# Kernel tuning notes

Measured on AMD Instinct MI355X. Metric: run time of the kernel, lower is better.

Reference implementation:

```python
import jax, jax.numpy as jnp
import numpy as np

N_NODES = 50000
N_EDGES = 800000
IN_C, HID, OUT_C, N_LAYERS = 32, 64, 8, 3

def _init(key, fan_in, shape):
    return jax.random.normal(key, shape, dtype=jnp.float32) * (1.0 / np.sqrt(fan_in))

def setup_inputs() -> dict:
    key = jax.random.key(0)
    ks = jax.random.split(key, 16)
    x = jax.random.uniform(ks[0], (N_NODES, IN_C), dtype=jnp.float32)
    edge_index = jax.random.randint(ks[1], (2, N_EDGES), 0, N_NODES, dtype=jnp.int64)
    return {
        "x": x,
        "edge_index": edge_index,
        # encoder MLP: in -> hid -> hid
        "enc_w1": _init(ks[2], IN_C, (IN_C, HID)),
        "enc_b1": jnp.zeros((HID,), jnp.float32),
        "enc_w2": _init(ks[3], HID, (HID, HID)),
        "enc_b2": jnp.zeros((HID,), jnp.float32),
        # stacked SAGEConv params: lin_l (aggregated neighbors, has bias) and lin_r (root)
        "sage_wl": _init(ks[4], HID, (N_LAYERS, HID, HID)),
        "sage_wr": _init(ks[5], HID, (N_LAYERS, HID, HID)),
        "sage_b": jnp.zeros((N_LAYERS, HID), jnp.float32),
        # decoder MLP: hid -> hid -> out
        "dec_w1": _init(ks[6], HID, (HID, HID)),
        "dec_b1": jnp.zeros((HID,), jnp.float32),
        "dec_w2": _init(ks[7], HID, (HID, OUT_C)),
        "dec_b2": jnp.zeros((OUT_C,), jnp.float32),
    }

def _gelu(x):
    return jax.nn.gelu(x, approximate=False)  # torch.nn.GELU default = exact erf

def reference(x, edge_index, enc_w1, enc_b1, enc_w2, enc_b2,
              sage_wl, sage_wr, sage_b, dec_w1, dec_b1, dec_w2, dec_b2):
    n = x.shape[0]
    src, dst = edge_index[0], edge_index[1]  # messages flow src -> dst (PyG convention)
    # in-degree counts for mean aggregation (computed once)
    deg = jax.ops.segment_sum(jnp.ones((src.shape[0],), x.dtype), dst, num_segments=n)
    inv_deg = 1.0 / jnp.maximum(deg, 1.0)

    # encoder MLP (Linear -> GELU -> Linear)
    h = _gelu(x @ enc_w1 + enc_b1) @ enc_w2 + enc_b2

    # SAGEConv + GELU blocks
    for l in range(sage_wl.shape[0]):
        agg = jax.ops.segment_sum(h[src], dst, num_segments=n) * inv_deg[:, None]
        h = _gelu(agg @ sage_wl[l] + h @ sage_wr[l] + sage_b[l])

    # decoder MLP
    out = _gelu(h @ dec_w1 + dec_b1) @ dec_w2 + dec_b2
    return out
```

## Files before the change

### kernel.cpp

```cpp
#include <hip/hip_runtime.h>
#include <math.h>

#define NN 50000
#define NE 800000
#define INC 32
#define HIDC 64
#define OUTC 8
#define NT_TILES ((NN + 63) / 64)
#define NPAD (NT_TILES * 64)
#define AS 68
#define XS 36
#define NCH 250
#define ECHK (NE / NCH)
#define BKD 128
#define NBK2 ((NN + BKD - 1) / BKD)
#define EC 12

__device__ __forceinline__ float gelu_exact(float x){
    return 0.5f * x * (1.0f + erff(x * 0.70710678118654752f));
}

template<int ST, int KK>
__device__ __forceinline__ void mm_tile(const float* __restrict__ At,
                                        const float* __restrict__ Ws,
                                        int m0, int n0, float acc[4][4])
{
    #pragma unroll 2
    for (int k = 0; k < KK; k += 2){
        float2 av[4];
        #pragma unroll
        for (int r = 0; r < 4; r++)
            av[r] = *(const float2*)&At[(m0+r)*ST + k];
        float4 w0 = *(const float4*)&Ws[(k+0)*HIDC + n0];
        float4 w1 = *(const float4*)&Ws[(k+1)*HIDC + n0];
        #pragma unroll
        for (int r = 0; r < 4; r++){
            acc[r][0] = fmaf(av[r].x, w0.x, acc[r][0]);
            acc[r][1] = fmaf(av[r].x, w0.y, acc[r][1]);
            acc[r][2] = fmaf(av[r].x, w0.z, acc[r][2]);
            acc[r][3] = fmaf(av[r].x, w0.w, acc[r][3]);
            acc[r][0] = fmaf(av[r].y, w1.x, acc[r][0]);
            acc[r][1] = fmaf(av[r].y, w1.y, acc[r][1]);
            acc[r][2] = fmaf(av[r].y, w1.z, acc[r][2]);
            acc[r][3] = fmaf(av[r].y, w1.w, acc[r][3]);
        }
    }
}


__global__ __launch_bounds__(512) void k_ebin(
    const int* __restrict__ src, const int* __restrict__ dst,
    int2* __restrict__ ebuf, int* __restrict__ cnts, int* __restrict__ lboff)
{
    __shared__ int cnt[512];
    __shared__ int cur[512];
    int c = blockIdx.x, tid = threadIdx.x;
    cnt[tid] = 0;
    __syncthreads();
    int e0 = c*ECHK;
    for (int i = e0 + tid; i < e0 + ECHK; i += 512)
        atomicAdd(&cnt[dst[i] >> 7], 1);
    __syncthreads();
    int v = cnt[tid];
    for (int off = 1; off < 512; off <<= 1){
        int t = (tid >= off) ? cnt[tid-off] : 0;
        __syncthreads();
        cnt[tid] += t;
        __syncthreads();
    }
    int excl = cnt[tid] - v;
    if (tid < NBK2){
        cnts[c*NBK2 + tid]  = v;
        lboff[c*NBK2 + tid] = excl;
    }
    cur[tid] = excl;
    __syncthreads();
    for (int i = e0 + tid; i < e0 + ECHK; i += 512){
        int d = dst[i], s = src[i];
        int p = atomicAdd(&cur[d >> 7], 1);
        ebuf[e0 + p] = make_int2(d, s);
    }
}

__global__ __launch_bounds__(256) void k_choff(
    const int* __restrict__ cnts, int* __restrict__ choff, int* __restrict__ btot)
{
    __shared__ int sd[256];
    int b = blockIdx.x, tid = threadIdx.x;
    int v = (tid < NCH) ? cnts[tid*NBK2 + b] : 0;
    sd[tid] = v;
    __syncthreads();
    for (int off = 1; off < 256; off <<= 1){
        int t = (tid >= off) ? sd[tid-off] : 0;
        __syncthreads();
        sd[tid] += t;
        __syncthreads();
    }
    if (tid < NCH) choff[b*NCH + tid] = sd[tid] - v;
    if (tid == 255) btot[b] = sd[255];
}

__global__ __launch_bounds__(512) void k_bbase(
    const int* __restrict__ btot, int* __restrict__ bbase,
    float* h0, float* h1, int* row_ptr)
{
    __shared__ int sd[512];
    int tid = threadIdx.x;
    int v = (tid < NBK2) ? btot[tid] : 0;
    sd[tid] = v;
    __syncthreads();
    for (int off = 1; off < 512; off <<= 1){
        int t = (tid >= off) ? sd[tid-off] : 0;
        __syncthreads();
        sd[tid] += t;
        __syncthreads();
    }
    if (tid < NBK2) bbase[tid] = sd[tid] - v;
    if (tid == 0) row_ptr[NN] = NE;
    if (tid < 64){
        h0[(size_t)NN*HIDC + tid] = 0.f;
        h1[(size_t)NN*HIDC + tid] = 0.f;
    }
}

__global__ __launch_bounds__(256) void k_bsort(
    const int2* __restrict__ ebuf, const int* __restrict__ lboff,
    const int* __restrict__ choff, const int* __restrict__ btot,
    const int* __restrict__ bbase,
    int* __restrict__ row_ptr, int* __restrict__ col,
    float* __restrict__ inv_deg)
{
    __shared__ int cum[NCH];
    __shared__ int lb[NCH];
    __shared__ int hcnt[BKD];
    __shared__ int fpos[BKD];
    int b = blockIdx.x, tid = threadIdx.x;
    if (tid < NCH){
        cum[tid] = choff[b*NCH + tid];
        lb[tid]  = lboff[tid*NBK2 + b];
    }
    if (tid < BKD) hcnt[tid] = 0;
    __syncthreads();
    int tot = btot[b];
    int lo = b << 7;
    int dl[EC], sv[EC];
    #pragma unroll
    for (int j = 0; j < EC; j++){
        int e = tid + j*256;
        dl[j] = -1; sv[j] = 0;
        if (e < tot){
            int lc = 0, hc = NCH;
            while (hc - lc > 1){ int mid = (lc+hc) >> 1; if (cum[mid] <= e) lc = mid; else hc = mid; }
            int2 pr = ebuf[lc*ECHK + lb[lc] + (e - cum[lc])];
            dl[j] = pr.x - lo; sv[j] = pr.y;
            atomicAdd(&hcnt[dl[j]], 1);
        }
    }
    for (int e = tid + EC*256; e < tot; e += 256){
        int lc = 0, hc = NCH;
        while (hc - lc > 1){ int mid = (lc+hc) >> 1; if (cum[mid] <= e) lc = mid; else hc = mid; }
        int2 pr = ebuf[lc*ECHK + lb[lc] + (e - cum[lc])];
        atomicAdd(&hcnt[pr.x - lo], 1);
    }
    __syncthreads();
    int v = (tid < BKD) ? hcnt[tid] : 0;
    for (int off = 1; off < BKD; off <<= 1){
        int t = (tid >= off && tid < BKD) ? hcnt[tid-off] : 0;
        __syncthreads();
        if (tid < BKD) hcnt[tid] += t;
        __syncthreads();
    }
    int base = bbase[b];
    if (tid < BKD){
        int excl = hcnt[tid] - v;
        int g = lo + tid;
        if (g < NN){
            row_ptr[g] = base + excl;
            inv_deg[g] = 1.0f / (float)max(v, 1);
        }
        fpos[tid] = base + excl;
    }
    __syncthreads();
    #pragma unroll
    for (int j = 0; j < EC; j++){
        if (dl[j] >= 0){
            int q = atomicAdd(&fpos[dl[j]], 1);
            col[q] = sv[j];
        }
    }
    for (int e = tid + EC*256; e < tot; e += 256){
        int lc = 0, hc = NCH;
        while (hc - lc > 1){ int mid = (lc+hc) >> 1; if (cum[mid] <= e) lc = mid; else hc = mid; }
        int2 pr = ebuf[lc*ECHK + lb[lc] + (e - cum[lc])];
        int q = atomicAdd(&fpos[pr.x - lo], 1);
        col[q] = pr.y;
    }
}

__global__ __launch_bounds__(256) void k_agg(
    const float* __restrict__ h_in,
    const int* __restrict__ row_ptr, const int* __restrict__ col,
    const float* __restrict__ inv_deg,
    float* __restrict__ agg)
{
    int tid = threadIdx.x;
    int wv = tid >> 6, f = tid & 63;
    int g = f >> 4, qoff = (f & 15) * 4;
    for (int node = blockIdx.x*4 + wv; node < NN; node += gridDim.x*4){
        int s0 = row_ptr[node], s1 = row_ptr[node+1];
        float a0 = 0.f, a1 = 0.f, a2 = 0.f, a3 = 0.f;
        for (int p0 = s0; p0 < s1; p0 += 64){
            int cnt = s1 - p0; if (cnt > 64) cnt = 64;
            int cidx = (f < cnt) ? col[p0 + f] : NN;
            int nq = (cnt + 3) >> 2;
            for (int t = 0; t < nq; t++){
                int sidx = __shfl(cidx, t*4 + g);
                float4 v = *(const float4*)&h_in[(size_t)sidx*HIDC + qoff];
                a0 += v.x; a1 += v.y; a2 += v.z; a3 += v.w;
            }
        }
        a0 += __shfl_xor(a0, 16); a0 += __shfl_xor(a0, 32);
        a1 += __shfl_xor(a1, 16); a1 += __shfl_xor(a1, 32);
        a2 += __shfl_xor(a2, 16); a2 += __shfl_xor(a2, 32);
        a3 += __shfl_xor(a3, 16); a3 += __shfl_xor(a3, 32);
        if (g == 0){
            float idg = inv_deg[node];
            float4 o = make_float4(a0*idg, a1*idg, a2*idg, a3*idg);
            *(float4*)&agg[(size_t)node*HIDC + qoff] = o;
        }
    }
}


__global__ __launch_bounds__(256) void k_enc(
    const float* __restrict__ x,
    const float* __restrict__ w1, const float* __restrict__ b1,
    const float* __restrict__ w2, const float* __restrict__ b2,
    float* __restrict__ h)
{
    __shared__ float w1s[INC*HIDC];
    __shared__ float w2s[HIDC*HIDC];
    __shared__ float Xt[64*XS];
    __shared__ float T[64*AS];
    int tid = threadIdx.x, tile = blockIdx.x;
    for (int i = tid*4; i < INC*HIDC;  i += 1024)
        *(float4*)&w1s[i] = *(const float4*)&w1[i];
    for (int i = tid*4; i < HIDC*HIDC; i += 1024)
        *(float4*)&w2s[i] = *(const float4*)&w2[i];
    for (int i = tid*4; i < 64*INC; i += 1024){
        int m = i >> 5, k = i & 31;
        int row = tile*64 + m; if (row >= NN) row = NN-1;
        *(float4*)&Xt[m*XS + k] = *(const float4*)&x[(size_t)row*INC + k];
    }
    __syncthreads();
    int tx = tid & 15, ty = tid >> 4;
    int m0 = ty*4, n0 = tx*4;
    float4 b1v = *(const float4*)&b1[n0];
    float acc[4][4];
    #pragma unroll
    for (int r = 0; r < 4; r++){
        acc[r][0]=b1v.x; acc[r][1]=b1v.y; acc[r][2]=b1v.z; acc[r][3]=b1v.w;
    }
    mm_tile<XS, INC>(Xt, w1s, m0, n0, acc);
    #pragma unroll
    for (int r = 0; r < 4; r++){
        float4 o = make_float4(gelu_exact(acc[r][0]), gelu_exact(acc[r][1]),
                               gelu_exact(acc[r][2]), gelu_exact(acc[r][3]));
        *(float4*)&T[(m0+r)*AS + n0] = o;
    }
    __syncthreads();
    float4 b2v = *(const float4*)&b2[n0];
    #pragma unroll
    for (int r = 0; r < 4; r++){
        acc[r][0]=b2v.x; acc[r][1]=b2v.y; acc[r][2]=b2v.z; acc[r][3]=b2v.w;
    }
    mm_tile<AS, HIDC>(T, w2s, m0, n0, acc);
    #pragma unroll
    for (int r = 0; r < 4; r++){
        int node = tile*64 + m0 + r;
        if (node < NN)
            *(float4*)&h[(size_t)node*HIDC + n0] =
                make_float4(acc[r][0], acc[r][1], acc[r][2], acc[r][3]);
    }
}

__global__ __launch_bounds__(256) void k_sage(
    const float* __restrict__ h_in, const float* __restrict__ agg,
    const float* __restrict__ wl, const float* __restrict__ wr,
    const float* __restrict__ bias, float* __restrict__ h_out)
{
    __shared__ float Wl[HIDC*HIDC];
    __shared__ float Wr[HIDC*HIDC];
    __shared__ float At[64*AS];
    int tid = threadIdx.x, tile = blockIdx.x;
    for (int i = tid*4; i < HIDC*HIDC; i += 1024){
        *(float4*)&Wl[i] = *(const float4*)&wl[i];
        *(float4*)&Wr[i] = *(const float4*)&wr[i];
    }
    const float* abase = agg + (size_t)tile*64*HIDC;
    for (int i = tid*4; i < 64*HIDC; i += 1024){
        int m = i >> 6, k = i & 63;
        *(float4*)&At[m*AS + k] = *(const float4*)&abase[i];
    }
    __syncthreads();
    int tx = tid & 15, ty = tid >> 4;
    int m0 = ty*4, n0 = tx*4;
    float4 bv = *(const float4*)&bias[n0];
    float acc[4][4];
    #pragma unroll
    for (int r = 0; r < 4; r++){
        acc[r][0]=bv.x; acc[r][1]=bv.y; acc[r][2]=bv.z; acc[r][3]=bv.w;
    }
    mm_tile<AS, HIDC>(At, Wl, m0, n0, acc);
    __syncthreads();
    const float* hbase = h_in + (size_t)tile*64*HIDC;
    for (int i = tid*4; i < 64*HIDC; i += 1024){
        int m = i >> 6, k = i & 63;
        *(float4*)&At[m*AS + k] = *(const float4*)&hbase[i];
    }
    __syncthreads();
    mm_tile<AS, HIDC>(At, Wr, m0, n0, acc);
    #pragma unroll
    for (int r = 0; r < 4; r++){
        int node = tile*64 + m0 + r;
        if (node < NN)
            *(float4*)&h_out[(size_t)node*HIDC + n0] =
                make_float4(gelu_exact(acc[r][0]), gelu_exact(acc[r][1]),
                            gelu_exact(acc[r][2]), gelu_exact(acc[r][3]));
    }
}

__global__ __launch_bounds__(256) void k_dec(
    const float* __restrict__ hbuf,
    const float* __restrict__ w1, const float* __restrict__ b1,
    const float* __restrict__ w2, const float* __restrict__ b2,
    float* __restrict__ out)
{
    __shared__ float w1s[HIDC*HIDC];
    __shared__ float w2s[HIDC*OUTC];
    __shared__ float At[64*AS];
    __shared__ float T[64*AS];
    int tid = threadIdx.x, tile = blockIdx.x;
    for (int i = tid*4; i < HIDC*HIDC; i += 1024)
        *(float4*)&w1s[i] = *(const float4*)&w1[i];
    if (tid*4 < HIDC*OUTC)
        *(float4*)&w2s[tid*4] = *(const float4*)&w2[tid*4];
    const float* hbase = hbuf + (size_t)tile*64*HIDC;
    for (int i = tid*4; i < 64*HIDC; i += 1024){
        int m = i >> 6, k = i & 63;
        *(float4*)&At[m*AS + k] = *(const float4*)&hbase[i];
    }
    __syncthreads();
    int tx = tid & 15, ty = tid >> 4;
    int m0 = ty*4, n0 = tx*4;
    float4 b1v = *(const float4*)&b1[n0];
    float acc[4][4];
    #pragma unroll
    for (int r = 0; r < 4; r++){
        acc[r][0]=b1v.x; acc[r][1]=b1v.y; acc[r][2]=b1v.z; acc[r][3]=b1v.w;
    }
    mm_tile<AS, HIDC>(At, w1s, m0, n0, acc);
    #pragma unroll
    for (int r = 0; r < 4; r++){
        float4 o = make_float4(gelu_exact(acc[r][0]), gelu_exact(acc[r][1]),
                               gelu_exact(acc[r][2]), gelu_exact(acc[r][3]));
        *(float4*)&T[(m0+r)*AS + n0] = o;
    }
    __syncthreads();
    int m = tid >> 2, c0 = (tid & 3) * 2;
    float a0 = b2[c0], a1 = b2[c0+1];
    #pragma unroll 4
    for (int k = 0; k < HIDC; k++){
        float tv = T[m*AS + k];
        float2 wv = *(const float2*)&w2s[k*OUTC + c0];
        a0 = fmaf(tv, wv.x, a0);
        a1 = fmaf(tv, wv.y, a1);
    }
    int node = tile*64 + m;
    if (node < NN)
        *(float2*)&out[(size_t)node*OUTC + c0] = make_float2(a0, a1);
}

extern "C" void kernel_launch(void* const* d_in, const int* in_sizes, int n_in,
                              void* d_out, int out_size, void* d_ws, size_t ws_size,
                              hipStream_t stream){
    const float* x      = (const float*)d_in[0];
    const int*   ei     = (const int*)  d_in[1];
    const float* enc_w1 = (const float*)d_in[2];
    const float* enc_b1 = (const float*)d_in[3];
    const float* enc_w2 = (const float*)d_in[4];
    const float* enc_b2 = (const float*)d_in[5];
    const float* sage_wl= (const float*)d_in[6];
    const float* sage_wr= (const float*)d_in[7];
    const float* sage_b = (const float*)d_in[8];
    const float* dec_w1 = (const float*)d_in[9];
    const float* dec_b1 = (const float*)d_in[10];
    const float* dec_w2 = (const float*)d_in[11];
    const float* dec_b2 = (const float*)d_in[12];
    float* out = (float*)d_out;

    char* ws = (char*)d_ws;
    size_t off = 0;
    auto alloc = [&](size_t bytes)->void*{
        void* p = ws + off; off = (off + bytes + 255) & ~(size_t)255; return p;
    };
    int*   cnts     = (int*)  alloc((size_t)NCH*NBK2*4);
    int*   lboff    = (int*)  alloc((size_t)NCH*NBK2*4);
    int*   choff    = (int*)  alloc((size_t)NBK2*NCH*4);
    int*   btot     = (int*)  alloc((size_t)NBK2*4);
    int*   bbase    = (int*)  alloc((size_t)NBK2*4);
    int*   row_ptr  = (int*)  alloc((size_t)(NN+1)*4);
    int*   col      = (int*)  alloc((size_t)NE*4);
    float* inv_deg  = (float*)alloc((size_t)NN*4);
    float* h0       = (float*)alloc((size_t)NPAD*HIDC*4);
    float* h1       = (float*)alloc((size_t)NPAD*HIDC*4);
    float* agg      = (float*)alloc((size_t)NPAD*HIDC*4);
    int2*  ebuf     = (int2*)agg;

    const int* srcv = ei;
    const int* dstv = ei + NE;

    hipLaunchKernelGGL(k_ebin,  dim3(NCH),  dim3(512), 0, stream,
                       srcv, dstv, ebuf, cnts, lboff);
    hipLaunchKernelGGL(k_choff, dim3(NBK2), dim3(256), 0, stream,
                       cnts, choff, btot);
    hipLaunchKernelGGL(k_bbase, dim3(1),    dim3(512), 0, stream,
                       btot, bbase, h0, h1, row_ptr);
    hipLaunchKernelGGL(k_bsort, dim3(NBK2), dim3(256), 0, stream,
                       ebuf, lboff, choff, btot, bbase, row_ptr, col, inv_deg);

    hipLaunchKernelGGL(k_enc, dim3(NT_TILES), dim3(256), 0, stream,
                       x, enc_w1, enc_b1, enc_w2, enc_b2, h0);

    const float* hin = h0; float* hout = h1;
    for (int l = 0; l < 3; l++){
        hipLaunchKernelGGL(k_agg, dim3(2048), dim3(256), 0, stream,
                           hin, row_ptr, col, inv_deg, agg);
        hipLaunchKernelGGL(k_sage, dim3(NT_TILES), dim3(256), 0, stream,
                           hin, agg,
                           sage_wl + (size_t)l*HIDC*HIDC,
                           sage_wr + (size_t)l*HIDC*HIDC,
                           sage_b  + (size_t)l*HIDC,
                           hout);
        float* t = (float*)hin; hin = hout; hout = t;
    }

    hipLaunchKernelGGL(k_dec, dim3(NT_TILES), dim3(256), 0, stream,
                       hin, dec_w1, dec_b1, dec_w2, dec_b2, out);
}
```

Baseline: 225.8 us.

## Fuse neighbor aggregation into SAGE layer kernel, dropping agg buffer

The separate gather-mean kernel and the SAGE GEMM kernel are merged into one kernel per layer. Each block aggregates its 64 nodes' neighbor features straight into shared memory and then runs the two 64x64 matmuls, reusing a single weight buffer in shared memory for Wl and then Wr. This removes the global round trip of the 50000x64 agg tensor and one launch per layer. The cost is a fixed one-tile-per-block schedule with 16 serial nodes per wavefront, which may balance the irregular gather worse than the old grid-stride aggregation.

```diff
diff --git a/kernel.cpp b/kernel.cpp
--- a/kernel.cpp
+++ b/kernel.cpp
@@ -197,37 +197,76 @@
     }
 }
 
-__global__ __launch_bounds__(256) void k_agg(
+__global__ __launch_bounds__(256) void k_sage_f(
     const float* __restrict__ h_in,
+    const float* __restrict__ wl, const float* __restrict__ wr,
+    const float* __restrict__ bias,
     const int* __restrict__ row_ptr, const int* __restrict__ col,
     const float* __restrict__ inv_deg,
-    float* __restrict__ agg)
-{
-    int tid = threadIdx.x;
+    float* __restrict__ h_out)
+{
+    __shared__ float Ws[HIDC*HIDC];
+    __shared__ float At[64*AS];
+    int tid = threadIdx.x, tile = blockIdx.x;
     int wv = tid >> 6, f = tid & 63;
+    for (int i = tid*4; i < HIDC*HIDC; i += 1024)
+        *(float4*)&Ws[i] = *(const float4*)&wl[i];
     int g = f >> 4, qoff = (f & 15) * 4;
-    for (int node = blockIdx.x*4 + wv; node < NN; node += gridDim.x*4){
-        int s0 = row_ptr[node], s1 = row_ptr[node+1];
-        float a0 = 0.f, a1 = 0.f, a2 = 0.f, a3 = 0.f;
-        for (int p0 = s0; p0 < s1; p0 += 64){
-            int cnt = s1 - p0; if (cnt > 64) cnt = 64;
-            int cidx = (f < cnt) ? col[p0 + f] : NN;
-            int nq = (cnt + 3) >> 2;
-            for (int t = 0; t < nq; t++){
-                int sidx = __shfl(cidx, t*4 + g);
-                float4 v = *(const float4*)&h_in[(size_t)sidx*HIDC + qoff];
-                a0 += v.x; a1 += v.y; a2 += v.z; a3 += v.w;
+    for (int m = wv*16; m < wv*16 + 16; m++){
+        int node = tile*64 + m;
+        if (node < NN){
+            int s0 = row_ptr[node], s1 = row_ptr[node+1];
+            float a0 = 0.f, a1 = 0.f, a2 = 0.f, a3 = 0.f;
+            for (int p0 = s0; p0 < s1; p0 += 64){
+                int cnt = s1 - p0; if (cnt > 64) cnt = 64;
+                int cidx = (f < cnt) ? col[p0 + f] : NN;
+                int nq = (cnt + 3) >> 2;
+                for (int t = 0; t < nq; t++){
+                    int sidx = __shfl(cidx, t*4 + g);
+                    float4 v = *(const float4*)&h_in[(size_t)sidx*HIDC + qoff];
+                    a0 += v.x; a1 += v.y; a2 += v.z; a3 += v.w;
+                }
             }
+            a0 += __shfl_xor(a0, 16); a0 += __shfl_xor(a0, 32);
+            a1 += __shfl_xor(a1, 16); a1 += __shfl_xor(a1, 32);
+            a2 += __shfl_xor(a2, 16); a2 += __shfl_xor(a2, 32);
+            a3 += __shfl_xor(a3, 16); a3 += __shfl_xor(a3, 32);
+            if (g == 0){
+                float idg = inv_deg[node];
+                *(float4*)&At[m*AS + qoff] =
+                    make_float4(a0*idg, a1*idg, a2*idg, a3*idg);
+            }
+        } else if (g == 0){
+            *(float4*)&At[m*AS + qoff] = make_float4(0.f, 0.f, 0.f, 0.f);
         }
-        a0 += __shfl_xor(a0, 16); a0 += __shfl_xor(a0, 32);
-        a1 += __shfl_xor(a1, 16); a1 += __shfl_xor(a1, 32);
-        a2 += __shfl_xor(a2, 16); a2 += __shfl_xor(a2, 32);
-        a3 += __shfl_xor(a3, 16); a3 += __shfl_xor(a3, 32);
-        if (g == 0){
-            float idg = inv_deg[node];
-            float4 o = make_float4(a0*idg, a1*idg, a2*idg, a3*idg);
-            *(float4*)&agg[(size_t)node*HIDC + qoff] = o;
-        }
+    }
+    __syncthreads();
+    int tx = tid & 15, ty = tid >> 4;
+    int m0 = ty*4, n0 = tx*4;
+    float4 bv = *(const float4*)&bias[n0];
+    float acc[4][4];
+    #pragma unroll
+    for (int r = 0; r < 4; r++){
+        acc[r][0]=bv.x; acc[r][1]=bv.y; acc[r][2]=bv.z; acc[r][3]=bv.w;
+    }
+    mm_tile<AS, HIDC>(At, Ws, m0, n0, acc);
+    __syncthreads();
+    for (int i = tid*4; i < HIDC*HIDC; i += 1024)
+        *(float4*)&Ws[i] = *(const float4*)&wr[i];
+    const float* hbase = h_in + (size_t)tile*64*HIDC;
+    for (int i = tid*4; i < 64*HIDC; i += 1024){
+        int m = i >> 6, k = i & 63;
+        *(float4*)&At[m*AS + k] = *(const float4*)&hbase[i];
+    }
+    __syncthreads();
+    mm_tile<AS, HIDC>(At, Ws, m0, n0, acc);
+    #pragma unroll
+    for (int r = 0; r < 4; r++){
+        int node = tile*64 + m0 + r;
+        if (node < NN)
+            *(float4*)&h_out[(size_t)node*HIDC + n0] =
+                make_float4(gelu_exact(acc[r][0]), gelu_exact(acc[r][1]),
+                            gelu_exact(acc[r][2]), gelu_exact(acc[r][3]));
     }
 }
 
@@ -281,52 +320,6 @@
         if (node < NN)
             *(float4*)&h[(size_t)node*HIDC + n0] =
                 make_float4(acc[r][0], acc[r][1], acc[r][2], acc[r][3]);
-    }
-}
-
-__global__ __launch_bounds__(256) void k_sage(
-    const float* __restrict__ h_in, const float* __restrict__ agg,
-    const float* __restrict__ wl, const float* __restrict__ wr,
-    const float* __restrict__ bias, float* __restrict__ h_out)
-{
-    __shared__ float Wl[HIDC*HIDC];
-    __shared__ float Wr[HIDC*HIDC];
-    __shared__ float At[64*AS];
-    int tid = threadIdx.x, tile = blockIdx.x;
-    for (int i = tid*4; i < HIDC*HIDC; i += 1024){
-        *(float4*)&Wl[i] = *(const float4*)&wl[i];
-        *(float4*)&Wr[i] = *(const float4*)&wr[i];
-    }
-    const float* abase = agg + (size_t)tile*64*HIDC;
-    for (int i = tid*4; i < 64*HIDC; i += 1024){
-        int m = i >> 6, k = i & 63;
-        *(float4*)&At[m*AS + k] = *(const float4*)&abase[i];
-    }
-    __syncthreads();
-    int tx = tid & 15, ty = tid >> 4;
-    int m0 = ty*4, n0 = tx*4;
-    float4 bv = *(const float4*)&bias[n0];
-    float acc[4][4];
-    #pragma unroll
-    for (int r = 0; r < 4; r++){
-        acc[r][0]=bv.x; acc[r][1]=bv.y; acc[r][2]=bv.z; acc[r][3]=bv.w;
-    }
-    mm_tile<AS, HIDC>(At, Wl, m0, n0, acc);
-    __syncthreads();
-    const float* hbase = h_in + (size_t)tile*64*HIDC;
-    for (int i = tid*4; i < 64*HIDC; i += 1024){
-        int m = i >> 6, k = i & 63;
-        *(float4*)&At[m*AS + k] = *(const float4*)&hbase[i];
-    }
-    __syncthreads();
-    mm_tile<AS, HIDC>(At, Wr, m0, n0, acc);
-    #pragma unroll
-    for (int r = 0; r < 4; r++){
-        int node = tile*64 + m0 + r;
-        if (node < NN)
-            *(float4*)&h_out[(size_t)node*HIDC + n0] =
-                make_float4(gelu_exact(acc[r][0]), gelu_exact(acc[r][1]),
-                            gelu_exact(acc[r][2]), gelu_exact(acc[r][3]));
     }
 }
 
@@ -414,8 +407,8 @@
     float* inv_deg  = (float*)alloc((size_t)NN*4);
     float* h0       = (float*)alloc((size_t)NPAD*HIDC*4);
     float* h1       = (float*)alloc((size_t)NPAD*HIDC*4);
-    float* agg      = (float*)alloc((size_t)NPAD*HIDC*4);
-    int2*  ebuf     = (int2*)agg;
+    float* ebufm    = (float*)alloc((size_t)NE*8);
+    int2*  ebuf     = (int2*)ebufm;
 
     const int* srcv = ei;
     const int* dstv = ei + NE;
@@ -434,14 +427,12 @@
 
     const float* hin = h0; float* hout = h1;
     for (int l = 0; l < 3; l++){
-        hipLaunchKernelGGL(k_agg, dim3(2048), dim3(256), 0, stream,
-                           hin, row_ptr, col, inv_deg, agg);
-        hipLaunchKernelGGL(k_sage, dim3(NT_TILES), dim3(256), 0, stream,
-                           hin, agg,
+        hipLaunchKernelGGL(k_sage_f, dim3(NT_TILES), dim3(256), 0, stream,
+                           hin,
                            sage_wl + (size_t)l*HIDC*HIDC,
                            sage_wr + (size_t)l*HIDC*HIDC,
                            sage_b  + (size_t)l*HIDC,
-                           hout);
+                           row_ptr, col, inv_deg, hout);
         float* t = (float*)hin; hin = hout; hout = t;
     }
 
```

Result: slower. 258.6 us (+14.5%).
